# Kernel optimization log

Hardware: AMD Instinct MI355X
Metric: run time of the kernel (lower is better)

## Reference

```python
import jax, jax.numpy as jnp
import numpy as np

NUM_HEADS, KEY_DIM, BLOCK, HALO = 8, 64, 8, 4
KV_KERNEL = BLOCK + 2 * HALO  # 16
EMB = NUM_HEADS * KEY_DIM     # 512


def setup_inputs() -> dict:
    key = jax.random.key(0)
    k = jax.random.split(key, 6)
    stddev = KEY_DIM ** -0.5
    return {
        "x": jax.random.normal(k[0], (8, 64, 64, 512), jnp.float32),
        "wq": jax.random.normal(k[1], (512, EMB), jnp.float32) * 0.02,
        "wkv": jax.random.normal(k[2], (512, 2 * EMB), jnp.float32) * 0.02,
        "wout": jax.random.normal(k[3], (EMB, EMB), jnp.float32) * 0.02,
        "pos_w": jax.random.normal(k[4], (KEY_DIM, 2 * KV_KERNEL - 1), jnp.float32) * stddev,
        "pos_h": jax.random.normal(k[5], (KEY_DIM, 2 * KV_KERNEL - 1), jnp.float32) * stddev,
    }


def rel_to_abs(rel):
    # rel: [B, N, hh, ww, 2*pos_dim-1] -> [B, N, hh, ww, pos_dim]
    b, n, hh, ww, dim = rel.shape
    pos_dim = (dim + 1) // 2
    gap = pos_dim - ww
    flat = rel.reshape(b, n, hh, ww * dim)[:, :, :, ww - 1:-1]
    return flat.reshape(b, n, hh, ww, 2 * (pos_dim - 1))[:, :, :, :, gap:pos_dim + gap]


def halo_forward(x, wq, wkv, wout, pos_w, pos_h):
    B, H, W, C = x.shape
    h, w = H // BLOCK, W // BLOCK
    K = KV_KERNEL
    scale = 1.0 / jnp.sqrt(jnp.asarray(KEY_DIM, x.dtype))

    # Query: [B, hd, h, w, block^2, key_dim]
    q = (x @ wq) * scale
    q = q.reshape(B, h, BLOCK, w, BLOCK, NUM_HEADS, KEY_DIM)
    attn_q = q.transpose(0, 5, 1, 3, 2, 4, 6).reshape(B, NUM_HEADS, h, w, BLOCK * BLOCK, KEY_DIM)

    # Overlapping halo KV windows (im2col-style gather, like tf.image.extract_patches)
    kv = x @ wkv
    kv_p = jnp.pad(kv, ((0, 0), (HALO, HALO), (HALO, HALO), (0, 0)))
    idx_h = jnp.arange(h)[:, None] * BLOCK + jnp.arange(K)[None, :]  # [h, K]
    idx_w = jnp.arange(w)[:, None] * BLOCK + jnp.arange(K)[None, :]  # [w, K]
    patches = kv_p[:, idx_h][:, :, :, idx_w]          # [B, h, K, w, K, 2*EMB]
    patches = patches.transpose(0, 1, 3, 2, 4, 5)     # [B, h, w, K, K, 2*EMB]
    patches = patches.reshape(B, h, w, K * K, NUM_HEADS, 2 * KEY_DIM)
    patches = patches.transpose(0, 4, 1, 2, 3, 5)     # [B, hd, h, w, K^2, 2*key_dim]
    key_t, val = patches[..., :KEY_DIM], patches[..., KEY_DIM:]

    scores = jnp.einsum('bnhwqc,bnhwkc->bnhwqk', attn_q, key_t)  # [B,hd,h,w,bq,bk]

    # Relative position logits (width + height), query already carries qk_scale
    pos_q = attn_q.reshape(B, NUM_HEADS * h * w, BLOCK, BLOCK, KEY_DIM)
    rel_w = rel_to_abs(pos_q @ pos_w)                                      # [B,N,hb,wb,K]
    rel_h = rel_to_abs(pos_q.transpose(0, 1, 3, 2, 4) @ pos_h)
    rel_h = rel_h.transpose(0, 1, 3, 2, 4)                                 # [B,N,hb,wb,K]
    pos = rel_w[..., None, :] + rel_h[..., :, None]                        # [B,N,hb,wb,Kh,Kw]
    pos = pos.reshape(B, NUM_HEADS, h, w, BLOCK * BLOCK, K * K)

    attn = jax.nn.softmax(scores + pos, axis=-1)
    out = jnp.einsum('bnhwqk,bnhwkc->bnhwqc', attn, val)
    out = out.reshape(B, NUM_HEADS, h, w, BLOCK, BLOCK, KEY_DIM)
    out = out.transpose(0, 2, 4, 3, 5, 1, 6).reshape(B, H, W, EMB)
    return out @ wout


def reference(x, wq, wkv, wout, pos_w, pos_h):
    return halo_forward(x, wq, wkv, wout, pos_w, pos_h)
```

## Files before the change

kernel.cpp:

```cpp
#include <hip/hip_runtime.h>
#include <hip/hip_fp16.h>
#include <math.h>

typedef _Float16 f16x8 __attribute__((ext_vector_type(8)));
typedef _Float16 f16x4 __attribute__((ext_vector_type(4)));
typedef float    f32x4 __attribute__((ext_vector_type(4)));

#define M_TOT 32768

__device__ __forceinline__ void gload16(const void* g, void* l) {
    __builtin_amdgcn_global_load_lds(
        (const __attribute__((address_space(1))) unsigned int*)g,
        (__attribute__((address_space(3))) unsigned int*)l, 16, 0, 0);
}

__global__ __launch_bounds__(256) void conv_x(const float* __restrict__ x,
                                              __half* __restrict__ y) {
    const size_t i = ((size_t)blockIdx.x * 256 + threadIdx.x) * 8;
    float4 a = *(const float4*)&x[i];
    float4 b = *(const float4*)&x[i + 4];
    __half2 h[4];
    h[0] = __floats2half2_rn(a.x, a.y);
    h[1] = __floats2half2_rn(a.z, a.w);
    h[2] = __floats2half2_rn(b.x, b.y);
    h[3] = __floats2half2_rn(b.z, b.w);
    *(float4*)&y[i] = *(float4*)h;
}

__global__ __launch_bounds__(256) void conv_w(const float* __restrict__ wq,
                                              const float* __restrict__ wkv,
                                              const float* __restrict__ wout,
                                              __half* __restrict__ wT,
                                              __half* __restrict__ woT) {
    const int id = blockIdx.x * 256 + threadIdx.x;
    const int nr = id >> 9, k = id & 511;
    if (nr < 512) {
        wT[(size_t)nr * 512 + k]  = __float2half(wq[k * 512 + nr] * 0.125f);
    } else if (nr < 1536) {
        wT[(size_t)nr * 512 + k]  = __float2half(wkv[k * 1024 + (nr - 512)]);
    } else {
        woT[(size_t)(nr - 1536) * 512 + k] = __float2half(wout[k * 512 + (nr - 1536)]);
    }
}

template <int MODE>
__global__ __launch_bounds__(256) void mfma_gemm(
    const __half* __restrict__ A, const __half* __restrict__ Bt,
    __half* __restrict__ q16, __half* __restrict__ k16, __half* __restrict__ vT,
    float* __restrict__ outf)
{
    __shared__ _Float16 As[128 * 32];
    __shared__ _Float16 Bs[128 * 32];

    const int t = threadIdx.x;
    const int l = t & 63, w = t >> 6;
    const int wr = w >> 1, wc = w & 1;
    const int bm = blockIdx.x, bn = blockIdx.y;

    f32x4 zero = {0.f, 0.f, 0.f, 0.f};
    f32x4 acc[4][4];
    #pragma unroll
    for (int i = 0; i < 4; ++i)
        #pragma unroll
        for (int j = 0; j < 4; ++j) acc[i][j] = zero;

    const int srow = w * 32 + (l >> 2);
    const int sch  = (l & 3) * 8;
    const size_t abase = (size_t)(bm * 128 + srow) * 512 + sch;
    const size_t bbase = (size_t)(bn * 128 + srow) * 512 + sch;
    _Float16* ldsA0 = &As[(w * 2 + 0) * 512];
    _Float16* ldsA1 = &As[(w * 2 + 1) * 512];
    _Float16* ldsB0 = &Bs[(w * 2 + 0) * 512];
    _Float16* ldsB1 = &Bs[(w * 2 + 1) * 512];

    const int lr = l & 15, lk = (l >> 4) * 8;

    for (int k0 = 0; k0 < 512; k0 += 32) {
        gload16(A  + abase + k0,            ldsA0);
        gload16(A  + abase + 16 * 512 + k0, ldsA1);
        gload16(Bt + bbase + k0,            ldsB0);
        gload16(Bt + bbase + 16 * 512 + k0, ldsB1);
        __syncthreads();

        f16x8 af[4], bf[4];
        #pragma unroll
        for (int i = 0; i < 4; ++i)
            af[i] = *(const f16x8*)&As[(wr * 64 + i * 16 + lr) * 32 + lk];
        #pragma unroll
        for (int j = 0; j < 4; ++j)
            bf[j] = *(const f16x8*)&Bs[(wc * 64 + j * 16 + lr) * 32 + lk];
        #pragma unroll
        for (int i = 0; i < 4; ++i)
            #pragma unroll
            for (int j = 0; j < 4; ++j)
                acc[i][j] = __builtin_amdgcn_mfma_f32_16x16x32_f16(af[i], bf[j], acc[i][j], 0, 0, 0);
        __syncthreads();
    }

    const int lq = l >> 4;
    #pragma unroll
    for (int i = 0; i < 4; ++i) {
        #pragma unroll
        for (int j = 0; j < 4; ++j) {
            const int row0 = bm * 128 + wr * 64 + i * 16 + lq * 4;
            const int col  = bn * 128 + wc * 64 + j * 16 + lr;
            if (MODE == 1) {
                #pragma unroll
                for (int r = 0; r < 4; ++r)
                    outf[(size_t)(row0 + r) * 512 + col] = acc[i][j][r];
            } else if (bn < 4) {
                #pragma unroll
                for (int r = 0; r < 4; ++r)
                    q16[(size_t)(row0 + r) * 512 + col] = __float2half(acc[i][j][r]);
            } else if (wc == 0) {
                const int head = bn - 4, d2 = j * 16 + lr;
                #pragma unroll
                for (int r = 0; r < 4; ++r)
                    k16[(size_t)(row0 + r) * 512 + head * 64 + d2] = __float2half(acc[i][j][r]);
            } else {
                const int head = bn - 4, d2 = j * 16 + lr;
                const int bb = row0 >> 12, pix = row0 & 4095;
                f16x4 pv;
                #pragma unroll
                for (int r = 0; r < 4; ++r) pv[r] = (_Float16)acc[i][j][r];
                *(f16x4*)(vT + ((size_t)((bb * 8 + head) * 64 + d2)) * 4096 + pix) = pv;
            }
        }
    }
}

__global__ __launch_bounds__(256, 3) void halo_attn(
    const __half* __restrict__ qbuf, const __half* __restrict__ kbuf,
    const __half* __restrict__ vT,
    const float* __restrict__ posw, const float* __restrict__ posh,
    const __half* __restrict__ zp,
    __half* __restrict__ obuf)
{
    __shared__ __align__(16) char KP[64 * 520];
    __shared__ float RWT[32][68];
    __shared__ float RHT[32][68];
    __shared__ float red[4][64];
    __shared__ float red2[4][64];

    const int hw = blockIdx.x;
    const int wg = (hw & 7) * 512 + (hw >> 3);
    const int wb = wg & 7, hb = (wg >> 3) & 7, n = (wg >> 6) & 7, b = wg >> 9;
    const int t = threadIdx.x;
    const int l = t & 63, g = t >> 6;
    const int hi = l >> 4, c15 = l & 15;

    f16x4 vfrag[16];
    {
        const __half* vrow = vT + ((size_t)((b * 8 + n) * 64 + g * 16 + c15)) * 4096;
        const int x0 = wb * 8 - 4 + hi * 4;
        const bool okx = (unsigned)x0 < 64u;
        #pragma unroll
        for (int kc = 0; kc < 16; ++kc) {
            const int y = hb * 8 - 4 + kc;
            const bool ok = okx && ((unsigned)y < 64u);
            const __half* p = ok ? (vrow + y * 64 + x0) : zp;
            vfrag[kc] = *(const f16x4*)p;
        }
    }

    for (int j5 = t; j5 < 4096; j5 += 256) {
        const int tb = j5 >> 11, idx = (j5 >> 6) & 31, d = j5 & 63;
        const float* src = tb ? posh : posw;
        const float v = (idx < 31) ? src[d * 31 + idx] : 0.f;
        *(__half*)(KP + tb * 4096 + ((idx * 128 + d * 2) ^ ((idx & 7) << 4))) = __float2half(v);
    }

    f16x8 qreg[4][2];
    #pragma unroll
    for (int qf = 0; qf < 4; ++qf) {
        const int q = qf * 16 + c15;
        const size_t pix = (size_t)((b * 64 + hb * 8 + (q >> 3)) * 64 + wb * 8 + (q & 7));
        #pragma unroll
        for (int dc = 0; dc < 2; ++dc)
            qreg[qf][dc] = *(const f16x8*)(qbuf + pix * 512 + n * 64 + dc * 32 + hi * 8);
    }
    __syncthreads();

    f32x4 accp[4];
    #pragma unroll
    for (int qf = 0; qf < 4; ++qf) accp[qf] = (f32x4){0.f, 0.f, 0.f, 0.f};
    {
        const int tb = g >> 1, ih = g & 1;
        const char* base = KP + tb * 4096;
        const int row = ih * 16 + c15;
        #pragma unroll
        for (int dc = 0; dc < 2; ++dc) {
            const int off = (row * 128 + dc * 64 + hi * 16) ^ ((row & 7) << 4);
            f16x8 a = *(const f16x8*)(base + off);
            #pragma unroll
            for (int qf = 0; qf < 4; ++qf)
                accp[qf] = __builtin_amdgcn_mfma_f32_16x16x32_f16(a, qreg[qf][dc], accp[qf], 0, 0, 0);
        }
    }
    __syncthreads();

    #pragma unroll
    for (int it = 0; it < 8; ++it) {
        const int cid = it * 256 + t;
        const int S = cid * 16;
        const int row = S >> 7;
        const int d0h = (((S & 127) >> 4) ^ (row & 7)) * 8;
        const int ky = hb * 8 - 4 + (row >> 4);
        const int kx = wb * 8 - 4 + (row & 15);
        const bool ok = ((unsigned)ky < 64u) && ((unsigned)kx < 64u);
        const __half* src = ok ? (kbuf + ((size_t)((b * 64 + ky) * 64 + kx)) * 512 + n * 64 + d0h)
                               : zp;
        gload16(src, KP + (it * 256 + g * 64) * 16);
    }

    {
        const int tb = g >> 1, ih = g & 1;
        float (*dst)[68] = tb ? RHT : RWT;
        #pragma unroll
        for (int qf = 0; qf < 4; ++qf)
            #pragma unroll
            for (int r = 0; r < 4; ++r)
                dst[ih * 16 + hi * 4 + r][qf * 16 + c15] = accp[qf][r];
    }
    __syncthreads();

    f32x4 accs[4][4];
    #pragma unroll
    for (int kf = 0; kf < 4; ++kf)
        #pragma unroll
        for (int qf = 0; qf < 4; ++qf) accs[kf][qf] = (f32x4){0.f, 0.f, 0.f, 0.f};

    #pragma unroll
    for (int kf = 0; kf < 4; ++kf) {
        const int row = g * 64 + kf * 16 + c15;
        #pragma unroll
        for (int dc = 0; dc < 2; ++dc) {
            const int off = (row * 128 + dc * 64 + hi * 16) ^ ((row & 7) << 4);
            f16x8 a = *(const f16x8*)(KP + off);
            #pragma unroll
            for (int qf = 0; qf < 4; ++qf)
                accs[kf][qf] = __builtin_amdgcn_mfma_f32_16x16x32_f16(a, qreg[qf][dc], accs[kf][qf], 0, 0, 0);
        }
    }

    float mq[4];
    #pragma unroll
    for (int qf = 0; qf < 4; ++qf) {
        const int q = qf * 16 + c15;
        const int qj = q & 7, qi = q >> 3;
        float pa[4], pb[4];
        #pragma unroll
        for (int r = 0; r < 4; ++r)  pa[r] = RWT[hi * 4 + r - qj + 15][q];
        #pragma unroll
        for (int kf = 0; kf < 4; ++kf) pb[kf] = RHT[g * 4 + kf - qi + 15][q];
        float mm = -1e30f;
        #pragma unroll
        for (int kf = 0; kf < 4; ++kf)
            #pragma unroll
            for (int r = 0; r < 4; ++r) {
                const float s = accs[kf][qf][r] + pa[r] + pb[kf];
                accs[kf][qf][r] = s;
                mm = fmaxf(mm, s);
            }
        mm = fmaxf(mm, __shfl_xor(mm, 16));
        mm = fmaxf(mm, __shfl_xor(mm, 32));
        mq[qf] = mm;
    }
    if (l < 16) {
        #pragma unroll
        for (int qf = 0; qf < 4; ++qf) red[g][qf * 16 + l] = mq[qf];
    }
    __syncthreads();

    float sums[4];
    #pragma unroll
    for (int qf = 0; qf < 4; ++qf) {
        const int q = qf * 16 + c15;
        const float mfull = fmaxf(fmaxf(red[0][q], red[1][q]), fmaxf(red[2][q], red[3][q]));
        float ss = 0.f;
        #pragma unroll
        for (int kf = 0; kf < 4; ++kf)
            #pragma unroll
            for (int r = 0; r < 4; ++r) {
                const float p = __expf(accs[kf][qf][r] - mfull);
                accs[kf][qf][r] = p;
                ss += p;
            }
        ss += __shfl_xor(ss, 16);
        ss += __shfl_xor(ss, 32);
        sums[qf] = ss;
        #pragma unroll
        for (int kf = 0; kf < 4; ++kf) {
            __half2 h01 = __floats2half2_rn(accs[kf][qf][0], accs[kf][qf][1]);
            __half2 h23 = __floats2half2_rn(accs[kf][qf][2], accs[kf][qf][3]);
            uint2 wv;
            wv.x = *(unsigned*)&h01;
            wv.y = *(unsigned*)&h23;
            *(uint2*)(KP + q * 520 + (g * 64 + kf * 16 + hi * 4) * 2) = wv;
        }
    }
    if (l < 16) {
        #pragma unroll
        for (int qf = 0; qf < 4; ++qf) red2[g][qf * 16 + l] = sums[qf];
    }
    __syncthreads();

    f32x4 acco[4];
    #pragma unroll
    for (int qf = 0; qf < 4; ++qf) acco[qf] = (f32x4){0.f, 0.f, 0.f, 0.f};
    #pragma unroll
    for (int kc = 0; kc < 16; ++kc) {
        const f16x4 bf = vfrag[kc];
        #pragma unroll
        for (int qf = 0; qf < 4; ++qf) {
            const f16x4 af = *(const f16x4*)(KP + (qf * 16 + c15) * 520 + (kc * 16 + hi * 4) * 2);
            acco[qf] = __builtin_amdgcn_mfma_f32_16x16x16f16(af, bf, acco[qf], 0, 0, 0);
        }
    }

    #pragma unroll
    for (int qf = 0; qf < 4; ++qf) {
        #pragma unroll
        for (int r = 0; r < 4; ++r) {
            const int q = qf * 16 + hi * 4 + r;
            const float den = red2[0][q] + red2[1][q] + red2[2][q] + red2[3][q];
            const float v = acco[qf][r] / den;
            const size_t pix = (size_t)((b * 64 + hb * 8 + (q >> 3)) * 64 + wb * 8 + (q & 7));
            obuf[pix * 512 + n * 64 + g * 16 + c15] = __float2half(v);
        }
    }
}

extern "C" void kernel_launch(void* const* d_in, const int* in_sizes, int n_in,
                              void* d_out, int out_size, void* d_ws, size_t ws_size,
                              hipStream_t stream)
{
    const float* x    = (const float*)d_in[0];
    const float* wq   = (const float*)d_in[1];
    const float* wkv  = (const float*)d_in[2];
    const float* wout = (const float*)d_in[3];
    const float* posw = (const float*)d_in[4];
    const float* posh = (const float*)d_in[5];
    float* out = (float*)d_out;

    const size_t NPIX = (size_t)M_TOT * 512;
    __half* x16 = (__half*)d_ws;
    __half* wT  = x16 + NPIX;
    __half* woT = wT + (size_t)1536 * 512;
    __half* q16 = woT + (size_t)512 * 512;
    __half* k16 = q16 + NPIX;
    __half* vT  = k16 + NPIX;
    __half* o16 = vT + NPIX;
    __half* zp  = o16 + NPIX;

    hipMemsetAsync(zp, 0, 256, stream);

    conv_x<<<(M_TOT * 512) / (256 * 8), 256, 0, stream>>>(x, x16);
    conv_w<<<(2048 * 512) / 256, 256, 0, stream>>>(wq, wkv, wout, wT, woT);

    dim3 g1(M_TOT / 128, 12);
    mfma_gemm<0><<<g1, 256, 0, stream>>>(x16, wT, q16, k16, vT, nullptr);

    halo_attn<<<4096, 256, 0, stream>>>(q16, k16, vT, posw, posh, zp, o16);

    dim3 g3(M_TOT / 128, 4);
    mfma_gemm<1><<<g3, 256, 0, stream>>>(o16, woT, nullptr, nullptr, nullptr, out);
}
```

Before: 227.2 us.

## Split halo attention queries across 8 waves per block

Doubles the halo_attn workgroup to 512 threads. The extra four waves split the 64 queries into two halves, so each wave holds half the query fragments, score accumulators and output accumulators. This cuts per-thread register pressure and adds parallelism per block. In exchange, each wave duplicates the V fragment loads and the position-logit MFMA work, and launch_bounds(512,3) may force register limits or spills.

Result: slower. 249.3 us (+9.7%).

```diff
diff --git a/kernel.cpp b/kernel.cpp
--- a/kernel.cpp
+++ b/kernel.cpp
@@ -129,7 +129,7 @@
     }
 }
 
-__global__ __launch_bounds__(256, 3) void halo_attn(
+__global__ __launch_bounds__(512, 3) void halo_attn(
     const __half* __restrict__ qbuf, const __half* __restrict__ kbuf,
     const __half* __restrict__ vT,
     const float* __restrict__ posw, const float* __restrict__ posh,
@@ -146,7 +146,8 @@
     const int wg = (hw & 7) * 512 + (hw >> 3);
     const int wb = wg & 7, hb = (wg >> 3) & 7, n = (wg >> 6) & 7, b = wg >> 9;
     const int t = threadIdx.x;
-    const int l = t & 63, g = t >> 6;
+    const int l = t & 63, w = t >> 6;
+    const int g = w & 3, h = w >> 2;
     const int hi = l >> 4, c15 = l & 15;
 
     f16x4 vfrag[16];
@@ -163,27 +164,27 @@
         }
     }
 
-    for (int j5 = t; j5 < 4096; j5 += 256) {
+    for (int j5 = t; j5 < 4096; j5 += 512) {
         const int tb = j5 >> 11, idx = (j5 >> 6) & 31, d = j5 & 63;
         const float* src = tb ? posh : posw;
         const float v = (idx < 31) ? src[d * 31 + idx] : 0.f;
         *(__half*)(KP + tb * 4096 + ((idx * 128 + d * 2) ^ ((idx & 7) << 4))) = __float2half(v);
     }
 
-    f16x8 qreg[4][2];
-    #pragma unroll
-    for (int qf = 0; qf < 4; ++qf) {
-        const int q = qf * 16 + c15;
+    f16x8 qreg[2][2];
+    #pragma unroll
+    for (int j = 0; j < 2; ++j) {
+        const int q = (h * 2 + j) * 16 + c15;
         const size_t pix = (size_t)((b * 64 + hb * 8 + (q >> 3)) * 64 + wb * 8 + (q & 7));
         #pragma unroll
         for (int dc = 0; dc < 2; ++dc)
-            qreg[qf][dc] = *(const f16x8*)(qbuf + pix * 512 + n * 64 + dc * 32 + hi * 8);
-    }
-    __syncthreads();
-
-    f32x4 accp[4];
-    #pragma unroll
-    for (int qf = 0; qf < 4; ++qf) accp[qf] = (f32x4){0.f, 0.f, 0.f, 0.f};
+            qreg[j][dc] = *(const f16x8*)(qbuf + pix * 512 + n * 64 + dc * 32 + hi * 8);
+    }
+    __syncthreads();
+
+    f32x4 accp[2];
+    accp[0] = (f32x4){0.f, 0.f, 0.f, 0.f};
+    accp[1] = accp[0];
     {
         const int tb = g >> 1, ih = g & 1;
         const char* base = KP + tb * 4096;
@@ -193,15 +194,15 @@
             const int off = (row * 128 + dc * 64 + hi * 16) ^ ((row & 7) << 4);
             f16x8 a = *(const f16x8*)(base + off);
             #pragma unroll
-            for (int qf = 0; qf < 4; ++qf)
-                accp[qf] = __builtin_amdgcn_mfma_f32_16x16x32_f16(a, qreg[qf][dc], accp[qf], 0, 0, 0);
-        }
-    }
-    __syncthreads();
-
-    #pragma unroll
-    for (int it = 0; it < 8; ++it) {
-        const int cid = it * 256 + t;
+            for (int j = 0; j < 2; ++j)
+                accp[j] = __builtin_amdgcn_mfma_f32_16x16x32_f16(a, qreg[j][dc], accp[j], 0, 0, 0);
+        }
+    }
+    __syncthreads();
+
+    #pragma unroll
+    for (int it = 0; it < 4; ++it) {
+        const int cid = it * 512 + t;
         const int S = cid * 16;
         const int row = S >> 7;
         const int d0h = (((S & 127) >> 4) ^ (row & 7)) * 8;
@@ -210,25 +211,25 @@
         const bool ok = ((unsigned)ky < 64u) && ((unsigned)kx < 64u);
         const __half* src = ok ? (kbuf + ((size_t)((b * 64 + ky) * 64 + kx)) * 512 + n * 64 + d0h)
                                : zp;
-        gload16(src, KP + (it * 256 + g * 64) * 16);
+        gload16(src, KP + (it * 512 + w * 64) * 16);
     }
 
     {
         const int tb = g >> 1, ih = g & 1;
         float (*dst)[68] = tb ? RHT : RWT;
         #pragma unroll
-        for (int qf = 0; qf < 4; ++qf)
+        for (int j = 0; j < 2; ++j)
             #pragma unroll
             for (int r = 0; r < 4; ++r)
-                dst[ih * 16 + hi * 4 + r][qf * 16 + c15] = accp[qf][r];
-    }
-    __syncthreads();
-
-    f32x4 accs[4][4];
+                dst[ih * 16 + hi * 4 + r][(h * 2 + j) * 16 + c15] = accp[j][r];
+    }
+    __syncthreads();
+
+    f32x4 accs[4][2];
     #pragma unroll
     for (int kf = 0; kf < 4; ++kf)
         #pragma unroll
-        for (int qf = 0; qf < 4; ++qf) accs[kf][qf] = (f32x4){0.f, 0.f, 0.f, 0.f};
+        for (int j = 0; j < 2; ++j) accs[kf][j] = (f32x4){0.f, 0.f, 0.f, 0.f};
 
     #pragma unroll
     for (int kf = 0; kf < 4; ++kf) {
@@ -238,15 +239,15 @@
             const int off = (row * 128 + dc * 64 + hi * 16) ^ ((row & 7) << 4);
             f16x8 a = *(const f16x8*)(KP + off);
             #pragma unroll
-            for (int qf = 0; qf < 4; ++qf)
-                accs[kf][qf] = __builtin_amdgcn_mfma_f32_16x16x32_f16(a, qreg[qf][dc], accs[kf][qf], 0, 0, 0);
-        }
-    }
-
-    float mq[4];
-    #pragma unroll
-    for (int qf = 0; qf < 4; ++qf) {
-        const int q = qf * 16 + c15;
+            for (int j = 0; j < 2; ++j)
+                accs[kf][j] = __builtin_amdgcn_mfma_f32_16x16x32_f16(a, qreg[j][dc], accs[kf][j], 0, 0, 0);
+        }
+    }
+
+    float mq[2];
+    #pragma unroll
+    for (int j = 0; j < 2; ++j) {
+        const int q = (h * 2 + j) * 16 + c15;
         const int qj = q & 7, qi = q >> 3;
         float pa[4], pb[4];
         #pragma unroll
@@ -258,41 +259,41 @@
         for (int kf = 0; kf < 4; ++kf)
             #pragma unroll
             for (int r = 0; r < 4; ++r) {
-                const float s = accs[kf][qf][r] + pa[r] + pb[kf];
-                accs[kf][qf][r] = s;
+                const float s = accs[kf][j][r] + pa[r] + pb[kf];
+                accs[kf][j][r] = s;
                 mm = fmaxf(mm, s);
             }
         mm = fmaxf(mm, __shfl_xor(mm, 16));
         mm = fmaxf(mm, __shfl_xor(mm, 32));
-        mq[qf] = mm;
+        mq[j] = mm;
     }
     if (l < 16) {
         #pragma unroll
-        for (int qf = 0; qf < 4; ++qf) red[g][qf * 16 + l] = mq[qf];
-    }
-    __syncthreads();
-
-    float sums[4];
-    #pragma unroll
-    for (int qf = 0; qf < 4; ++qf) {
-        const int q = qf * 16 + c15;
+        for (int j = 0; j < 2; ++j) red[g][(h * 2 + j) * 16 + l] = mq[j];
+    }
+    __syncthreads();
+
+    float sums[2];
+    #pragma unroll
+    for (int j = 0; j < 2; ++j) {
+        const int q = (h * 2 + j) * 16 + c15;
         const float mfull = fmaxf(fmaxf(red[0][q], red[1][q]), fmaxf(red[2][q], red[3][q]));
         float ss = 0.f;
         #pragma unroll
         for (int kf = 0; kf < 4; ++kf)
             #pragma unroll
             for (int r = 0; r < 4; ++r) {
-                const float p = __expf(accs[kf][qf][r] - mfull);
-                accs[kf][qf][r] = p;
+                const float p = __expf(accs[kf][j][r] - mfull);
+                accs[kf][j][r] = p;
                 ss += p;
             }
         ss += __shfl_xor(ss, 16);
         ss += __shfl_xor(ss, 32);
-        sums[qf] = ss;
+        sums[j] = ss;
         #pragma unroll
         for (int kf = 0; kf < 4; ++kf) {
-            __half2 h01 = __floats2half2_rn(accs[kf][qf][0], accs[kf][qf][1]);
-            __half2 h23 = __floats2half2_rn(accs[kf][qf][2], accs[kf][qf][3]);
+            __half2 h01 = __floats2half2_rn(accs[kf][j][0], accs[kf][j][1]);
+            __half2 h23 = __floats2half2_rn(accs[kf][j][2], accs[kf][j][3]);
             uint2 wv;
             wv.x = *(unsigned*)&h01;
             wv.y = *(unsigned*)&h23;
@@ -301,30 +302,30 @@
     }
     if (l < 16) {
         #pragma unroll
-        for (int qf = 0; qf < 4; ++qf) red2[g][qf * 16 + l] = sums[qf];
-    }
-    __syncthreads();
-
-    f32x4 acco[4];
-    #pragma unroll
-    for (int qf = 0; qf < 4; ++qf) acco[qf] = (f32x4){0.f, 0.f, 0.f, 0.f};
+        for (int j = 0; j < 2; ++j) red2[g][(h * 2 + j) * 16 + l] = sums[j];
+    }
+    __syncthreads();
+
+    f32x4 acco[2];
+    acco[0] = (f32x4){0.f, 0.f, 0.f, 0.f};
+    acco[1] = acco[0];
     #pragma unroll
     for (int kc = 0; kc < 16; ++kc) {
         const f16x4 bf = vfrag[kc];
         #pragma unroll
-        for (int qf = 0; qf < 4; ++qf) {
-            const f16x4 af = *(const f16x4*)(KP + (qf * 16 + c15) * 520 + (kc * 16 + hi * 4) * 2);
-            acco[qf] = __builtin_amdgcn_mfma_f32_16x16x16f16(af, bf, acco[qf], 0, 0, 0);
-        }
-    }
-
-    #pragma unroll
-    for (int qf = 0; qf < 4; ++qf) {
+        for (int j = 0; j < 2; ++j) {
+            const f16x4 af = *(const f16x4*)(KP + ((h * 2 + j) * 16 + c15) * 520 + (kc * 16 + hi * 4) * 2);
+            acco[j] = __builtin_amdgcn_mfma_f32_16x16x16f16(af, bf, acco[j], 0, 0, 0);
+        }
+    }
+
+    #pragma unroll
+    for (int j = 0; j < 2; ++j) {
         #pragma unroll
         for (int r = 0; r < 4; ++r) {
-            const int q = qf * 16 + hi * 4 + r;
+            const int q = (h * 2 + j) * 16 + hi * 4 + r;
             const float den = red2[0][q] + red2[1][q] + red2[2][q] + red2[3][q];
-            const float v = acco[qf][r] / den;
+            const float v = acco[j][r] / den;
             const size_t pix = (size_t)((b * 64 + hb * 8 + (q >> 3)) * 64 + wb * 8 + (q & 7));
             obuf[pix * 512 + n * 64 + g * 16 + c15] = __float2half(v);
         }
@@ -361,7 +362,7 @@
     dim3 g1(M_TOT / 128, 12);
     mfma_gemm<0><<<g1, 256, 0, stream>>>(x16, wT, q16, k16, vT, nullptr);
 
-    halo_attn<<<4096, 256, 0, stream>>>(q16, k16, vT, posw, posh, zp, o16);
+    halo_attn<<<4096, 512, 0, stream>>>(q16, k16, vT, posw, posh, zp, o16);
 
     dim3 g3(M_TOT / 128, 4);
     mfma_gemm<1><<<g3, 256, 0, stream>>>(o16, woT, nullptr, nullptr, nullptr, out);
```

## Pad transposed V rows to drop bounds checks and use K=32 MFMA for PV

Applied to the files above, without the earlier changes.

V is now stored transposed with a zero border of four columns on each side of every 64-wide row (stride 72). A new small kernel zeroes these borders. The attention kernel can then load 8-wide V fragments without per-x bounds checks and run the P·V product with the 16x16x32 MFMA instead of the 16x16x16 one, halving the MFMA count. The K-tile global-to-LDS load is issued before the position-table setup so it overlaps it, which needs a separate LDS buffer for the position tables. The cost is an extra launch, slightly more workspace, and a wider LDS row stride.

New measurement: 228.0 us. Within noise of the previous version (+0.3%).

```diff
diff --git a/kernel.cpp b/kernel.cpp
--- a/kernel.cpp
+++ b/kernel.cpp
@@ -7,6 +7,7 @@
 typedef float    f32x4 __attribute__((ext_vector_type(4)));
 
 #define M_TOT 32768
+#define VROW  4608
 
 __device__ __forceinline__ void gload16(const void* g, void* l) {
     __builtin_amdgcn_global_load_lds(
@@ -43,10 +44,18 @@
     }
 }
 
+__global__ __launch_bounds__(256) void vborder(__half* __restrict__ vTp) {
+    const int id = blockIdx.x * 256 + threadIdx.x;
+    const int row = id >> 7, rem = id & 127;
+    const int y = rem >> 1, side = rem & 1;
+    f16x4 z = {(_Float16)0.f, (_Float16)0.f, (_Float16)0.f, (_Float16)0.f};
+    *(f16x4*)(vTp + (size_t)row * VROW + y * 72 + side * 68) = z;
+}
+
 template <int MODE>
 __global__ __launch_bounds__(256) void mfma_gemm(
     const __half* __restrict__ A, const __half* __restrict__ Bt,
-    __half* __restrict__ q16, __half* __restrict__ k16, __half* __restrict__ vT,
+    __half* __restrict__ q16, __half* __restrict__ k16, __half* __restrict__ vTp,
     float* __restrict__ outf)
 {
     __shared__ _Float16 As[128 * 32];
@@ -120,10 +129,11 @@
             } else {
                 const int head = bn - 4, d2 = j * 16 + lr;
                 const int bb = row0 >> 12, pix = row0 & 4095;
+                const int py = pix >> 6, px = pix & 63;
                 f16x4 pv;
                 #pragma unroll
                 for (int r = 0; r < 4; ++r) pv[r] = (_Float16)acc[i][j][r];
-                *(f16x4*)(vT + ((size_t)((bb * 8 + head) * 64 + d2)) * 4096 + pix) = pv;
+                *(f16x4*)(vTp + ((size_t)((bb * 8 + head) * 64 + d2)) * VROW + py * 72 + px + 4) = pv;
             }
         }
     }
@@ -131,16 +141,18 @@
 
 __global__ __launch_bounds__(256, 3) void halo_attn(
     const __half* __restrict__ qbuf, const __half* __restrict__ kbuf,
-    const __half* __restrict__ vT,
+    const __half* __restrict__ vTp,
     const float* __restrict__ posw, const float* __restrict__ posh,
     const __half* __restrict__ zp,
     __half* __restrict__ obuf)
 {
-    __shared__ __align__(16) char KP[64 * 520];
-    __shared__ float RWT[32][68];
-    __shared__ float RHT[32][68];
+    __shared__ __align__(16) char KP[64 * 528];
+    __shared__ __align__(16) char PTRW[17408];
     __shared__ float red[4][64];
     __shared__ float red2[4][64];
+
+    float (*RWT)[68] = (float(*)[68])PTRW;
+    float (*RHT)[68] = (float(*)[68])(PTRW + 8704);
 
     const int hw = blockIdx.x;
     const int wg = (hw & 7) * 512 + (hw >> 3);
@@ -148,56 +160,6 @@
     const int t = threadIdx.x;
     const int l = t & 63, g = t >> 6;
     const int hi = l >> 4, c15 = l & 15;
-
-    f16x4 vfrag[16];
-    {
-        const __half* vrow = vT + ((size_t)((b * 8 + n) * 64 + g * 16 + c15)) * 4096;
-        const int x0 = wb * 8 - 4 + hi * 4;
-        const bool okx = (unsigned)x0 < 64u;
-        #pragma unroll
-        for (int kc = 0; kc < 16; ++kc) {
-            const int y = hb * 8 - 4 + kc;
-            const bool ok = okx && ((unsigned)y < 64u);
-            const __half* p = ok ? (vrow + y * 64 + x0) : zp;
-            vfrag[kc] = *(const f16x4*)p;
-        }
-    }
-
-    for (int j5 = t; j5 < 4096; j5 += 256) {
-        const int tb = j5 >> 11, idx = (j5 >> 6) & 31, d = j5 & 63;
-        const float* src = tb ? posh : posw;
-        const float v = (idx < 31) ? src[d * 31 + idx] : 0.f;
-        *(__half*)(KP + tb * 4096 + ((idx * 128 + d * 2) ^ ((idx & 7) << 4))) = __float2half(v);
-    }
-
-    f16x8 qreg[4][2];
-    #pragma unroll
-    for (int qf = 0; qf < 4; ++qf) {
-        const int q = qf * 16 + c15;
-        const size_t pix = (size_t)((b * 64 + hb * 8 + (q >> 3)) * 64 + wb * 8 + (q & 7));
-        #pragma unroll
-        for (int dc = 0; dc < 2; ++dc)
-            qreg[qf][dc] = *(const f16x8*)(qbuf + pix * 512 + n * 64 + dc * 32 + hi * 8);
-    }
-    __syncthreads();
-
-    f32x4 accp[4];
-    #pragma unroll
-    for (int qf = 0; qf < 4; ++qf) accp[qf] = (f32x4){0.f, 0.f, 0.f, 0.f};
-    {
-        const int tb = g >> 1, ih = g & 1;
-        const char* base = KP + tb * 4096;
-        const int row = ih * 16 + c15;
-        #pragma unroll
-        for (int dc = 0; dc < 2; ++dc) {
-            const int off = (row * 128 + dc * 64 + hi * 16) ^ ((row & 7) << 4);
-            f16x8 a = *(const f16x8*)(base + off);
-            #pragma unroll
-            for (int qf = 0; qf < 4; ++qf)
-                accp[qf] = __builtin_amdgcn_mfma_f32_16x16x32_f16(a, qreg[qf][dc], accp[qf], 0, 0, 0);
-        }
-    }
-    __syncthreads();
 
     #pragma unroll
     for (int it = 0; it < 8; ++it) {
@@ -213,6 +175,55 @@
         gload16(src, KP + (it * 256 + g * 64) * 16);
     }
 
+    f16x8 vfrag[8];
+    {
+        const __half* vrow = vTp + ((size_t)((b * 8 + n) * 64 + g * 16 + c15)) * VROW;
+        const int xoff = wb * 8 + (hi & 1) * 8;
+        #pragma unroll
+        for (int kc = 0; kc < 8; ++kc) {
+            const int ki = kc * 2 + (hi >> 1);
+            const int y = hb * 8 - 4 + ki;
+            const __half* p = ((unsigned)y < 64u) ? (vrow + y * 72 + xoff) : zp;
+            vfrag[kc] = *(const f16x8*)p;
+        }
+    }
+
+    for (int j5 = t; j5 < 4096; j5 += 256) {
+        const int tb = j5 >> 11, idx = (j5 >> 6) & 31, d = j5 & 63;
+        const float* src = tb ? posh : posw;
+        const float v = (idx < 31) ? src[d * 31 + idx] : 0.f;
+        *(__half*)(PTRW + tb * 4096 + ((idx * 128 + d * 2) ^ ((idx & 7) << 4))) = __float2half(v);
+    }
+
+    f16x8 qreg[4][2];
+    #pragma unroll
+    for (int qf = 0; qf < 4; ++qf) {
+        const int q = qf * 16 + c15;
+        const size_t pix = (size_t)((b * 64 + hb * 8 + (q >> 3)) * 64 + wb * 8 + (q & 7));
+        #pragma unroll
+        for (int dc = 0; dc < 2; ++dc)
+            qreg[qf][dc] = *(const f16x8*)(qbuf + pix * 512 + n * 64 + dc * 32 + hi * 8);
+    }
+    __syncthreads();
+
+    f32x4 accp[4];
+    #pragma unroll
+    for (int qf = 0; qf < 4; ++qf) accp[qf] = (f32x4){0.f, 0.f, 0.f, 0.f};
+    {
+        const int tb = g >> 1, ih = g & 1;
+        const char* base = PTRW + tb * 4096;
+        const int row = ih * 16 + c15;
+        #pragma unroll
+        for (int dc = 0; dc < 2; ++dc) {
+            const int off = (row * 128 + dc * 64 + hi * 16) ^ ((row & 7) << 4);
+            f16x8 a = *(const f16x8*)(base + off);
+            #pragma unroll
+            for (int qf = 0; qf < 4; ++qf)
+                accp[qf] = __builtin_amdgcn_mfma_f32_16x16x32_f16(a, qreg[qf][dc], accp[qf], 0, 0, 0);
+        }
+    }
+    __syncthreads();
+
     {
         const int tb = g >> 1, ih = g & 1;
         float (*dst)[68] = tb ? RHT : RWT;
@@ -296,7 +307,7 @@
             uint2 wv;
             wv.x = *(unsigned*)&h01;
             wv.y = *(unsigned*)&h23;
-            *(uint2*)(KP + q * 520 + (g * 64 + kf * 16 + hi * 4) * 2) = wv;
+            *(uint2*)(KP + q * 528 + (g * 64 + kf * 16 + hi * 4) * 2) = wv;
         }
     }
     if (l < 16) {
@@ -309,12 +320,12 @@
     #pragma unroll
     for (int qf = 0; qf < 4; ++qf) acco[qf] = (f32x4){0.f, 0.f, 0.f, 0.f};
     #pragma unroll
-    for (int kc = 0; kc < 16; ++kc) {
-        const f16x4 bf = vfrag[kc];
+    for (int kc = 0; kc < 8; ++kc) {
+        const f16x8 bf = vfrag[kc];
         #pragma unroll
         for (int qf = 0; qf < 4; ++qf) {
-            const f16x4 af = *(const f16x4*)(KP + (qf * 16 + c15) * 520 + (kc * 16 + hi * 4) * 2);
-            acco[qf] = __builtin_amdgcn_mfma_f32_16x16x16f16(af, bf, acco[qf], 0, 0, 0);
+            const f16x8 af = *(const f16x8*)(KP + (qf * 16 + c15) * 528 + kc * 64 + hi * 16);
+            acco[qf] = __builtin_amdgcn_mfma_f32_16x16x32_f16(af, bf, acco[qf], 0, 0, 0);
         }
     }
 
@@ -344,24 +355,26 @@
     float* out = (float*)d_out;
 
     const size_t NPIX = (size_t)M_TOT * 512;
+    const size_t NVTP = (size_t)64 * 64 * VROW;
     __half* x16 = (__half*)d_ws;
     __half* wT  = x16 + NPIX;
     __half* woT = wT + (size_t)1536 * 512;
     __half* q16 = woT + (size_t)512 * 512;
     __half* k16 = q16 + NPIX;
-    __half* vT  = k16 + NPIX;
-    __half* o16 = vT + NPIX;
+    __half* vTp = k16 + NPIX;
+    __half* o16 = vTp + NVTP;
     __half* zp  = o16 + NPIX;
 
     hipMemsetAsync(zp, 0, 256, stream);
 
     conv_x<<<(M_TOT * 512) / (256 * 8), 256, 0, stream>>>(x, x16);
     conv_w<<<(2048 * 512) / 256, 256, 0, stream>>>(wq, wkv, wout, wT, woT);
+    vborder<<<2048, 256, 0, stream>>>(vTp);
 
     dim3 g1(M_TOT / 128, 12);
-    mfma_gemm<0><<<g1, 256, 0, stream>>>(x16, wT, q16, k16, vT, nullptr);
-
-    halo_attn<<<4096, 256, 0, stream>>>(q16, k16, vT, posw, posh, zp, o16);
+    mfma_gemm<0><<<g1, 256, 0, stream>>>(x16, wT, q16, k16, vTp, nullptr);
+
+    halo_attn<<<4096, 256, 0, stream>>>(q16, k16, vTp, posw, posh, zp, o16);
 
     dim3 g3(M_TOT / 128, 4);
     mfma_gemm<1><<<g3, 256, 0, stream>>>(o16, woT, nullptr, nullptr, nullptr, out);
```
